# Kernel tuning notes

Hardware: AMD Instinct MI355X
Metric: run time of the kernel (lower is better)

## Reference

```python
import jax, jax.numpy as jnp
import numpy as np
import math

EPS = 1e-5
B, S, D = 4, 4096, 2048


def setup_inputs() -> dict:
    key = jax.random.key(0)
    x = jax.random.normal(key, (B, S, D, 2), dtype=jnp.float32)  # complex x as (real, imag)
    g = jnp.array([1.0 / math.sqrt(2.0), 0.0, 1.0 / math.sqrt(2.0)], dtype=jnp.float32)
    gamma = jnp.tile(g[None, :], (D, 1))            # (D,3), torch init
    beta = jnp.zeros((D, 2), dtype=jnp.float32)     # complex beta as (real, imag)
    return {"x": x, "gamma": gamma, "beta": beta}


def reference(x, gamma, beta):
    b, s, d, _ = x.shape
    bs = b * s
    # complex mean over hidden dim == per-channel mean of real/imag
    x = x - jnp.mean(x, axis=2, keepdims=True)
    xr = x.reshape(bs, d, 2)
    # per-token 2x2 covariance of (real, imag)
    var = jnp.einsum('kdi,kdj->kij', xr, xr) / (d - 1)          # (bs,2,2)
    var = var + EPS * jnp.eye(2, dtype=x.dtype)
    w, v = jnp.linalg.eigh(var)                                  # (bs,2), (bs,2,2)
    inv_sqrt_w = 1.0 / jnp.sqrt(w)
    # std_inv = V diag(1/sqrt(w)) V^{-1}
    std_inv = jnp.einsum('kij,kj,kjl->kil', v, inv_sqrt_w, jnp.linalg.inv(v))
    # whiten: (bs,2,2) @ (bs,2,d) -> (bs,2,d)
    xw = jnp.einsum('kij,kdj->kid', std_inv, xr)
    # d-major flatten exactly as torch permute(2,0,1).reshape(d*bs,2,1)
    xf = jnp.transpose(xw, (2, 0, 1)).reshape(d * bs, 2)
    # per-dim symmetric 2x2 affine: [[g0,g1],[g1,g2]]
    G = jnp.stack([gamma[:, :2], gamma[:, 1:]], axis=-1)         # (d,2,2)
    Gt = jnp.tile(G, (bs, 1, 1))                                 # (d*bs,2,2): element k -> G[k % d]
    y = jnp.einsum('kij,kj->ki', Gt, xf)                         # (d*bs,2)
    y = jnp.transpose(y.reshape(d, bs, 2), (1, 0, 2)) + beta[None, :, :]  # (bs,d,2)
    return y.reshape(b, s, d, 2)
```

## Files before the change

kernel.cpp:

```cpp
#include <hip/hip_runtime.h>


constexpr int D = 2048;
constexpr int THREADS = 256;
constexpr float EPSV = 1e-5f;

__global__ __launch_bounds__(THREADS)
void spectral_ln_kernel(const float* __restrict__ x,
                        const float* __restrict__ gamma,
                        const float* __restrict__ beta,
                        float* __restrict__ out)
{
    const int k = blockIdx.x;
    const int t = threadIdx.x;
    const long base = (long)k * (D * 2);

    const float4* __restrict__ xin = (const float4*)(x + base);
    float4 v[4];
#pragma unroll
    for (int j = 0; j < 4; ++j) v[j] = xin[t * 4 + j];

    float sr = 0.f, si = 0.f;
#pragma unroll
    for (int j = 0; j < 4; ++j) { sr += v[j].x + v[j].z; si += v[j].y + v[j].w; }
#pragma unroll
    for (int o = 32; o > 0; o >>= 1) {
        sr += __shfl_xor(sr, o, 64);
        si += __shfl_xor(si, o, 64);
    }
    __shared__ float red[4][3];
    const int wid = t >> 6, lane = t & 63;
    if (lane == 0) { red[wid][0] = sr; red[wid][1] = si; }
    __syncthreads();
    const float mu_r = (red[0][0] + red[1][0] + red[2][0] + red[3][0]) * (1.0f / D);
    const float mu_i = (red[0][1] + red[1][1] + red[2][1] + red[3][1]) * (1.0f / D);
    __syncthreads();

    float rr = 0.f, ri = 0.f, ii = 0.f;
#pragma unroll
    for (int j = 0; j < 4; ++j) {
        v[j].x -= mu_r; v[j].y -= mu_i; v[j].z -= mu_r; v[j].w -= mu_i;
        rr += v[j].x * v[j].x + v[j].z * v[j].z;
        ri += v[j].x * v[j].y + v[j].z * v[j].w;
        ii += v[j].y * v[j].y + v[j].w * v[j].w;
    }
#pragma unroll
    for (int o = 32; o > 0; o >>= 1) {
        rr += __shfl_xor(rr, o, 64);
        ri += __shfl_xor(ri, o, 64);
        ii += __shfl_xor(ii, o, 64);
    }
    if (lane == 0) { red[wid][0] = rr; red[wid][1] = ri; red[wid][2] = ii; }
    __syncthreads();
    const float inv_dm1 = 1.0f / (D - 1);
    const float a = (red[0][0] + red[1][0] + red[2][0] + red[3][0]) * inv_dm1 + EPSV;
    const float b = (red[0][1] + red[1][1] + red[2][1] + red[3][1]) * inv_dm1;
    const float c = (red[0][2] + red[1][2] + red[2][2] + red[3][2]) * inv_dm1 + EPSV;

    const float s   = sqrtf(a * c - b * b);
    const float tt  = sqrtf(a + c + 2.f * s);
    const float inv = 1.f / (s * tt);
    const float si00 = (c + s) * inv;
    const float si01 = -b * inv;
    const float si11 = (a + s) * inv;

    const int m = k & (D - 1);
    const float g0 = gamma[m * 3 + 0];
    const float g1 = gamma[m * 3 + 1];
    const float g2 = gamma[m * 3 + 2];
    const float M00 = g0 * si00 + g1 * si01;
    const float M01 = g0 * si01 + g1 * si11;
    const float M10 = g1 * si00 + g2 * si01;
    const float M11 = g1 * si01 + g2 * si11;

    const float4* __restrict__ bp = (const float4*)beta;
    float4* __restrict__ op = (float4*)(out + base);
#pragma unroll
    for (int j = 0; j < 4; ++j) {
        const float4 bt = bp[t * 4 + j];
        float4 o4;
        o4.x = M00 * v[j].x + M01 * v[j].y + bt.x;
        o4.y = M10 * v[j].x + M11 * v[j].y + bt.y;
        o4.z = M00 * v[j].z + M01 * v[j].w + bt.z;
        o4.w = M10 * v[j].z + M11 * v[j].w + bt.w;
        op[t * 4 + j] = o4;
    }
}

extern "C" void kernel_launch(void* const* d_in, const int* in_sizes, int n_in,
                              void* d_out, int out_size, void* d_ws, size_t ws_size,
                              hipStream_t stream) {
    const float* x     = (const float*)d_in[0];
    const float* gamma = (const float*)d_in[1];
    const float* beta  = (const float*)d_in[2];
    float* out = (float*)d_out;
    const int n_tokens = in_sizes[0] / (D * 2);
    spectral_ln_kernel<<<dim3(n_tokens), dim3(THREADS), 0, stream>>>(x, gamma, beta, out);
}
```

Baseline: 441.3 us.

## Map one wavefront per token with single-pass moment reduction

Each 64-lane wavefront now handles a whole token, so a block covers four tokens. The shared-memory reductions and block barriers go away, and the accesses are coalesced with a j*64+lane stride. The mean and covariance are computed in one pass from raw sums (sum, sum of squares, cross sum) and the mean is subtracted only when writing the output. This costs more registers per thread (16 float4) and can lose precision through cancellation in the one-pass variance.

```diff
diff --git a/kernel.cpp b/kernel.cpp
--- a/kernel.cpp
+++ b/kernel.cpp
@@ -2,98 +2,84 @@
 
 
 constexpr int D = 2048;
-constexpr int THREADS = 256;
 constexpr float EPSV = 1e-5f;
 
-__global__ __launch_bounds__(THREADS)
-void spectral_ln_kernel(const float* __restrict__ x,
+__global__ __launch_bounds__(256)
+void spectral_ln_kernel(const float4* __restrict__ x4,
                         const float* __restrict__ gamma,
-                        const float* __restrict__ beta,
-                        float* __restrict__ out)
+                        const float4* __restrict__ beta4,
+                        float4* __restrict__ out4,
+                        int n_tokens)
 {
-    const int k = blockIdx.x;
-    const int t = threadIdx.x;
-    const long base = (long)k * (D * 2);
+    const int lane = threadIdx.x & 63;
+    const int wid  = threadIdx.x >> 6;
+    const int tok  = blockIdx.x * 4 + wid;
+    if (tok >= n_tokens) return;
+    const long base = (long)tok * (D * 2 / 4);
 
-    const float4* __restrict__ xin = (const float4*)(x + base);
-    float4 v[4];
+    const float4* __restrict__ xin = x4 + base;
+    float4 v[16];
 #pragma unroll
-    for (int j = 0; j < 4; ++j) v[j] = xin[t * 4 + j];
+    for (int j = 0; j < 16; ++j) v[j] = xin[j * 64 + lane];
 
-    float sr = 0.f, si = 0.f;
+    float sr = 0.f, si = 0.f, rr = 0.f, ri = 0.f, ii = 0.f;
 #pragma unroll
-    for (int j = 0; j < 4; ++j) { sr += v[j].x + v[j].z; si += v[j].y + v[j].w; }
-#pragma unroll
-    for (int o = 32; o > 0; o >>= 1) {
-        sr += __shfl_xor(sr, o, 64);
-        si += __shfl_xor(si, o, 64);
-    }
-    __shared__ float red[4][3];
-    const int wid = t >> 6, lane = t & 63;
-    if (lane == 0) { red[wid][0] = sr; red[wid][1] = si; }
-    __syncthreads();
-    const float mu_r = (red[0][0] + red[1][0] + red[2][0] + red[3][0]) * (1.0f / D);
-    const float mu_i = (red[0][1] + red[1][1] + red[2][1] + red[3][1]) * (1.0f / D);
-    __syncthreads();
-
-    float rr = 0.f, ri = 0.f, ii = 0.f;
-#pragma unroll
-    for (int j = 0; j < 4; ++j) {
-        v[j].x -= mu_r; v[j].y -= mu_i; v[j].z -= mu_r; v[j].w -= mu_i;
+    for (int j = 0; j < 16; ++j) {
+        sr += v[j].x + v[j].z;  si += v[j].y + v[j].w;
         rr += v[j].x * v[j].x + v[j].z * v[j].z;
         ri += v[j].x * v[j].y + v[j].z * v[j].w;
         ii += v[j].y * v[j].y + v[j].w * v[j].w;
     }
 #pragma unroll
     for (int o = 32; o > 0; o >>= 1) {
+        sr += __shfl_xor(sr, o, 64);
+        si += __shfl_xor(si, o, 64);
         rr += __shfl_xor(rr, o, 64);
         ri += __shfl_xor(ri, o, 64);
         ii += __shfl_xor(ii, o, 64);
     }
-    if (lane == 0) { red[wid][0] = rr; red[wid][1] = ri; red[wid][2] = ii; }
-    __syncthreads();
-    const float inv_dm1 = 1.0f / (D - 1);
-    const float a = (red[0][0] + red[1][0] + red[2][0] + red[3][0]) * inv_dm1 + EPSV;
-    const float b = (red[0][1] + red[1][1] + red[2][1] + red[3][1]) * inv_dm1;
-    const float c = (red[0][2] + red[1][2] + red[2][2] + red[3][2]) * inv_dm1 + EPSV;
+
+    const float invD = 1.0f / D, inv_dm1 = 1.0f / (D - 1);
+    const float mu_r = sr * invD, mu_i = si * invD;
+    const float a = (rr - sr * mu_r) * inv_dm1 + EPSV;
+    const float b = (ri - sr * mu_i) * inv_dm1;
+    const float c = (ii - si * mu_i) * inv_dm1 + EPSV;
 
     const float s   = sqrtf(a * c - b * b);
-    const float tt  = sqrtf(a + c + 2.f * s);
-    const float inv = 1.f / (s * tt);
-    const float si00 = (c + s) * inv;
-    const float si01 = -b * inv;
-    const float si11 = (a + s) * inv;
+    const float t2  = sqrtf(a + c + 2.f * s);
+    const float inv = 1.f / (s * t2);
+    const float si00 = (c + s) * inv, si01 = -b * inv, si11 = (a + s) * inv;
 
-    const int m = k & (D - 1);
-    const float g0 = gamma[m * 3 + 0];
-    const float g1 = gamma[m * 3 + 1];
-    const float g2 = gamma[m * 3 + 2];
+    const int m = tok & (D - 1);
+    const float g0 = gamma[m * 3 + 0], g1 = gamma[m * 3 + 1], g2 = gamma[m * 3 + 2];
     const float M00 = g0 * si00 + g1 * si01;
     const float M01 = g0 * si01 + g1 * si11;
     const float M10 = g1 * si00 + g2 * si01;
     const float M11 = g1 * si01 + g2 * si11;
 
-    const float4* __restrict__ bp = (const float4*)beta;
-    float4* __restrict__ op = (float4*)(out + base);
+    float4* __restrict__ op = out4 + base;
 #pragma unroll
-    for (int j = 0; j < 4; ++j) {
-        const float4 bt = bp[t * 4 + j];
+    for (int j = 0; j < 16; ++j) {
+        const float4 bt = beta4[j * 64 + lane];
+        const float cr0 = v[j].x - mu_r, ci0 = v[j].y - mu_i;
+        const float cr1 = v[j].z - mu_r, ci1 = v[j].w - mu_i;
         float4 o4;
-        o4.x = M00 * v[j].x + M01 * v[j].y + bt.x;
-        o4.y = M10 * v[j].x + M11 * v[j].y + bt.y;
-        o4.z = M00 * v[j].z + M01 * v[j].w + bt.z;
-        o4.w = M10 * v[j].z + M11 * v[j].w + bt.w;
-        op[t * 4 + j] = o4;
+        o4.x = M00 * cr0 + M01 * ci0 + bt.x;
+        o4.y = M10 * cr0 + M11 * ci0 + bt.y;
+        o4.z = M00 * cr1 + M01 * ci1 + bt.z;
+        o4.w = M10 * cr1 + M11 * ci1 + bt.w;
+        op[j * 64 + lane] = o4;
     }
 }
 
 extern "C" void kernel_launch(void* const* d_in, const int* in_sizes, int n_in,
                               void* d_out, int out_size, void* d_ws, size_t ws_size,
                               hipStream_t stream) {
-    const float* x     = (const float*)d_in[0];
-    const float* gamma = (const float*)d_in[1];
-    const float* beta  = (const float*)d_in[2];
-    float* out = (float*)d_out;
+    const float4* x4    = (const float4*)d_in[0];
+    const float*  gamma = (const float*)d_in[1];
+    const float4* beta4 = (const float4*)d_in[2];
+    float4* out4 = (float4*)d_out;
     const int n_tokens = in_sizes[0] / (D * 2);
-    spectral_ln_kernel<<<dim3(n_tokens), dim3(THREADS), 0, stream>>>(x, gamma, beta, out);
+    const int blocks = (n_tokens + 3) / 4;
+    spectral_ln_kernel<<<dim3(blocks), dim3(256), 0, stream>>>(x4, gamma, beta4, out4, n_tokens);
 }
```

New measurement: 435.4 us. About the same (-1.3%).
